# Optimization experiments

Hardware: AMD Instinct MI355X
Metric: run time of the kernel (lower is better)

Reference implementation:

```python
import jax, jax.numpy as jnp
import numpy as np
import math

D_MODEL = 1024
N_HEADS = 16
D_HEAD = D_MODEL // N_HEADS
WINDOW_LEN = 128
DILATION = 4
SEQ = 3072
BATCH = 1


def setup_inputs() -> dict:
    key = jax.random.key(0)
    ks = jax.random.split(key, 10)
    def xavier(k, shape):
        fan_out, fan_in = shape
        lim = math.sqrt(6.0 / (fan_in + fan_out))
        return jax.random.uniform(k, shape, jnp.float32, -lim, lim)
    return {
        "x": jax.random.normal(ks[0], (SEQ, BATCH, D_MODEL), jnp.float32),
        "beta": 0.1 * jax.random.normal(ks[1], (N_HEADS,), jnp.float32),
        "Wq": xavier(ks[2], (D_MODEL, D_MODEL)),
        "bq": jnp.zeros((D_MODEL,), jnp.float32),
        "Wk": xavier(ks[3], (D_MODEL, D_MODEL)),
        "bk": jnp.zeros((D_MODEL,), jnp.float32),
        "Wv": xavier(ks[4], (D_MODEL, D_MODEL)),
        "bv": jnp.zeros((D_MODEL,), jnp.float32),
        "Wo": xavier(ks[5], (D_MODEL, D_MODEL)),
        "bo": jnp.zeros((D_MODEL,), jnp.float32),
    }


def _causal_windowed_bias(seq_len):
    # allowed iff 0 <= (i-j), (i-j)//dilation < window_len, (i-j) % dilation == 0
    idx = jnp.arange(seq_len)
    diff = idx[:, None] - idx[None, :]
    allowed = (diff >= 0) & (diff // DILATION < WINDOW_LEN) & (diff % DILATION == 0)
    return jnp.where(allowed, 0.0, -jnp.inf).astype(jnp.float32)  # [S, S]


def reference(x, beta, Wq, bq, Wk, bk, Wv, bv, Wo, bo):
    s, b, d = x.shape
    # projections: nn.Linear => x @ W.T + b
    def split_heads(t):  # [s, b, h*dh] -> [b, h, s, dh]
        return t.reshape(s, b, N_HEADS, D_HEAD).transpose(1, 2, 0, 3)
    q = split_heads(x @ Wq.T + bq)
    k = split_heads(x @ Wk.T + bk)
    v = split_heads(x @ Wv.T + bv)
    # beta scaling folded into q, attention uses scale=1.0
    q = q / (math.sqrt(D_HEAD) * jnp.exp(beta)[None, :, None, None])
    bias = _causal_windowed_bias(s)  # [S, S]
    scores = jnp.einsum('bhsd,bhtd->bhst', q, k) + bias
    attn = jax.nn.softmax(scores, axis=-1)
    ctx = jnp.einsum('bhst,bhtd->bhsd', attn, v)  # [b, h, s, dh]
    ctx = ctx.transpose(2, 0, 1, 3).reshape(s, b, d)  # [s, b, d_model]
    return ctx @ Wo.T + bo
```

## Files before the change

kernel.cpp:

```cpp
#include <hip/hip_runtime.h>
#include <math.h>

#define SEQ   3072
#define DM    1024
#define NH    16
#define DH    64
#define WIN   128
#define DIL   4
#define TSUB  768

typedef __attribute__((ext_vector_type(8))) short    short8;
typedef __attribute__((ext_vector_type(8))) _Float16 half8;
typedef __attribute__((ext_vector_type(4))) float    floatx4;

__device__ __forceinline__ float bf2f(unsigned short u) {
    return __uint_as_float(((unsigned)u) << 16);
}
__device__ __forceinline__ unsigned short f2bf(float f) {
    unsigned u = __float_as_uint(f);
    return (unsigned short)((u + 0x7FFFu + ((u >> 16) & 1u)) >> 16);
}
__device__ __forceinline__ unsigned short f2h(float f) {
    _Float16 h = (_Float16)f;
    return __builtin_bit_cast(unsigned short, h);
}

__device__ __forceinline__ void gload_lds16(const void* g, void* l) {
    __builtin_amdgcn_global_load_lds(
        (const __attribute__((address_space(1))) void*)g,
        (__attribute__((address_space(3))) void*)l, 16, 0, 0);
}

__global__ __launch_bounds__(256) void convert_kernel(
    const float* __restrict__ x,  const float* __restrict__ Wq,
    const float* __restrict__ Wk, const float* __restrict__ Wv,
    const float* __restrict__ Wo,
    ushort* __restrict__ xb,  ushort* __restrict__ Wqb,
    ushort* __restrict__ Wkb, ushort* __restrict__ Wvb,
    ushort* __restrict__ Wob)
{
    const float* s; ushort* d; int n;
    switch (blockIdx.y) {
        case 0: s = x;  d = xb;  n = SEQ * DM; break;
        case 1: s = Wq; d = Wqb; n = DM * DM;  break;
        case 2: s = Wk; d = Wkb; n = DM * DM;  break;
        case 3: s = Wv; d = Wvb; n = DM * DM;  break;
        default: s = Wo; d = Wob; n = DM * DM; break;
    }
    int i = (blockIdx.x * 256 + threadIdx.x) * 4;
    if (i >= n) return;
    float4 v = *(const float4*)&s[i];
    ushort4 o = { f2bf(v.x), f2bf(v.y), f2bf(v.z), f2bf(v.w) };
    *(ushort4*)&d[i] = o;
}

struct QkvSmem {
    ushort As[128][64];
    ushort Bs[64][64];
};

template<bool QSCALE>
__device__ __forceinline__ void gemm_qkv_body(QkvSmem& sm,
                                              const ushort* __restrict__ A,
                                              const ushort* __restrict__ W,
                                              const float* __restrict__ bias,
                                              const float* __restrict__ beta,
                                              ushort* __restrict__ C,
                                              int bx, int by)
{
    const int tid  = threadIdx.x;
    const int lane = tid & 63, w = tid >> 6;
    const int ln15 = lane & 15, quad = lane >> 4;
    const int wm = w >> 1, wn = w & 1;

    const int arow = tid >> 1;
    const int sh   = tid & 1;
    const int ska  = (arow >> 1) & 7;
    const ushort* aG = A + (size_t)(by * 128 + arow) * DM + sh * 32;
    ushort* aL[4];
#pragma unroll
    for (int c = 0; c < 4; ++c) {
        int pos = (4 * sh + c) ^ ska;
        aL[c] = &sm.As[arow][pos * 8];
    }

    const int brow = tid >> 2;
    const int sq   = tid & 3;
    const int skb  = (brow >> 1) & 7;
    const ushort* bG = W + (size_t)(bx * 64 + brow) * DM + sq * 16;
    ushort* bL[2];
#pragma unroll
    for (int c = 0; c < 2; ++c) {
        int pos = (2 * sq + c) ^ skb;
        bL[c] = &sm.Bs[brow][pos * 8];
    }

    const floatx4 zero = {0.f, 0.f, 0.f, 0.f};
    floatx4 acc[4][2];
#pragma unroll
    for (int i = 0; i < 4; ++i)
#pragma unroll
        for (int j = 0; j < 2; ++j) acc[i][j] = zero;

    short8 ra[4], rb[2];
#pragma unroll
    for (int c = 0; c < 4; ++c) ra[c] = *(const short8*)(aG + 8 * c);
#pragma unroll
    for (int c = 0; c < 2; ++c) rb[c] = *(const short8*)(bG + 8 * c);
#pragma unroll
    for (int c = 0; c < 4; ++c) *(short8*)aL[c] = ra[c];
#pragma unroll
    for (int c = 0; c < 2; ++c) *(short8*)bL[c] = rb[c];
    __syncthreads();

    const int rf = (ln15 >> 1) & 7;
#pragma unroll 2
    for (int k = 0; k < 16; ++k) {
        if (k < 15) {
            const ushort* aN = aG + (k + 1) * 64;
            const ushort* bN = bG + (k + 1) * 64;
#pragma unroll
            for (int c = 0; c < 4; ++c) ra[c] = *(const short8*)(aN + 8 * c);
#pragma unroll
            for (int c = 0; c < 2; ++c) rb[c] = *(const short8*)(bN + 8 * c);
        }
#pragma unroll
        for (int s = 0; s < 2; ++s) {
            short8 af[4], bf[2];
#pragma unroll
            for (int i = 0; i < 4; ++i)
                af[i] = *(const short8*)&sm.As[wm * 64 + i * 16 + ln15][((s * 4 + quad) ^ rf) * 8];
#pragma unroll
            for (int j = 0; j < 2; ++j)
                bf[j] = *(const short8*)&sm.Bs[wn * 32 + j * 16 + ln15][((s * 4 + quad) ^ rf) * 8];
#pragma unroll
            for (int i = 0; i < 4; ++i)
#pragma unroll
                for (int j = 0; j < 2; ++j)
                    acc[i][j] = __builtin_amdgcn_mfma_f32_16x16x32_bf16(af[i], bf[j], acc[i][j], 0, 0, 0);
        }
        __syncthreads();
        if (k < 15) {
#pragma unroll
            for (int c = 0; c < 4; ++c) *(short8*)aL[c] = ra[c];
#pragma unroll
            for (int c = 0; c < 2; ++c) *(short8*)bL[c] = rb[c];
        }
        __syncthreads();
    }

#pragma unroll
    for (int j = 0; j < 2; ++j) {
        const int col = bx * 64 + wn * 32 + j * 16 + ln15;
        const float b = bias[col];
        const float scale = QSCALE ? 0.125f * __expf(-beta[col >> 6]) : 1.0f;
#pragma unroll
        for (int i = 0; i < 4; ++i) {
            const int row0 = by * 128 + wm * 64 + i * 16 + quad * 4;
#pragma unroll
            for (int rg = 0; rg < 4; ++rg) {
                float vv = (acc[i][j][rg] + b) * scale;
                C[(size_t)(row0 + rg) * DM + col] = f2bf(vv);
            }
        }
    }
}

__global__ __launch_bounds__(256, 4) void qkv_kernel(
    const ushort* __restrict__ xb,
    const ushort* __restrict__ Wqb, const float* __restrict__ bq,
    const ushort* __restrict__ Wkb, const float* __restrict__ bk,
    const ushort* __restrict__ Wvb, const float* __restrict__ bv,
    const float* __restrict__ beta,
    ushort* __restrict__ q, ushort* __restrict__ k, ushort* __restrict__ v)
{
    __shared__ QkvSmem sm;
    const int z = blockIdx.z;
    const ushort* W = (z == 0) ? Wqb : (z == 1) ? Wkb : Wvb;
    const float*  b = (z == 0) ? bq  : (z == 1) ? bk  : bv;
    ushort*       C = (z == 0) ? q   : (z == 1) ? k   : v;
    if (z == 0)
        gemm_qkv_body<true >(sm, xb, W, b, beta, C, blockIdx.x, blockIdx.y);
    else
        gemm_qkv_body<false>(sm, xb, W, b, nullptr, C, blockIdx.x, blockIdx.y);
}

__global__ __launch_bounds__(256) void out_kernel(
    const ushort* __restrict__ ctxb, const ushort* __restrict__ Wob,
    const float* __restrict__ bo, float* __restrict__ out)
{
    __shared__ ushort As[64][64];
    __shared__ ushort Bs[64][64];

    const int tid  = threadIdx.x;
    const int lane = tid & 63, w = tid >> 6;
    const int ln15 = lane & 15, quad = lane >> 4;
    const int wm = w >> 1, wn = w & 1;
    const int bx = blockIdx.x, by = blockIdx.y;

    const int srow = tid >> 2;
    const int sq   = tid & 3;
    const int sk   = (srow >> 1) & 7;
    const ushort* aG = ctxb + (size_t)(by * 64 + srow) * DM + sq * 16;
    const ushort* bG = Wob  + (size_t)(bx * 64 + srow) * DM + sq * 16;
    ushort* aL[2]; ushort* bL[2];
#pragma unroll
    for (int c = 0; c < 2; ++c) {
        int pos = (2 * sq + c) ^ sk;
        aL[c] = &As[srow][pos * 8];
        bL[c] = &Bs[srow][pos * 8];
    }

    const floatx4 zero = {0.f, 0.f, 0.f, 0.f};
    floatx4 acc[2][2];
#pragma unroll
    for (int i = 0; i < 2; ++i)
#pragma unroll
        for (int j = 0; j < 2; ++j) acc[i][j] = zero;

    short8 ra[2], rb[2];
#pragma unroll
    for (int c = 0; c < 2; ++c) {
        ra[c] = *(const short8*)(aG + 8 * c);
        rb[c] = *(const short8*)(bG + 8 * c);
    }
#pragma unroll
    for (int c = 0; c < 2; ++c) { *(short8*)aL[c] = ra[c]; *(short8*)bL[c] = rb[c]; }
    __syncthreads();

    const int rf = (ln15 >> 1) & 7;
#pragma unroll 2
    for (int k = 0; k < 16; ++k) {
        if (k < 15) {
            const ushort* aN = aG + (k + 1) * 64;
            const ushort* bN = bG + (k + 1) * 64;
#pragma unroll
            for (int c = 0; c < 2; ++c) {
                ra[c] = *(const short8*)(aN + 8 * c);
                rb[c] = *(const short8*)(bN + 8 * c);
            }
        }
#pragma unroll
        for (int s = 0; s < 2; ++s) {
            short8 af[2], bf[2];
#pragma unroll
            for (int i = 0; i < 2; ++i)
                af[i] = *(const short8*)&As[wm * 32 + i * 16 + ln15][((s * 4 + quad) ^ rf) * 8];
#pragma unroll
            for (int j = 0; j < 2; ++j)
                bf[j] = *(const short8*)&Bs[wn * 32 + j * 16 + ln15][((s * 4 + quad) ^ rf) * 8];
#pragma unroll
            for (int i = 0; i < 2; ++i)
#pragma unroll
                for (int j = 0; j < 2; ++j)
                    acc[i][j] = __builtin_amdgcn_mfma_f32_16x16x32_bf16(af[i], bf[j], acc[i][j], 0, 0, 0);
        }
        __syncthreads();
        if (k < 15) {
#pragma unroll
            for (int c = 0; c < 2; ++c) { *(short8*)aL[c] = ra[c]; *(short8*)bL[c] = rb[c]; }
        }
        __syncthreads();
    }

#pragma unroll
    for (int j = 0; j < 2; ++j) {
        const int col = bx * 64 + wn * 32 + j * 16 + ln15;
        const float b = bo[col];
#pragma unroll
        for (int i = 0; i < 2; ++i) {
            const int row0 = by * 64 + wm * 32 + i * 16 + quad * 4;
#pragma unroll
            for (int rg = 0; rg < 4; ++rg)
                out[(size_t)(row0 + rg) * DM + col] = acc[i][j][rg] + b;
        }
    }
}

struct AttnSmem {
    union {
        ushort Ks[192 * 64];
        ushort Vt[6 * 4 * 64 * 8];
    } u;
    float S[32][195];
    float Rsum[32];
};

__global__ __launch_bounds__(256) void attn_kernel(
    const ushort* __restrict__ q, const ushort* __restrict__ k,
    const ushort* __restrict__ v, ushort* __restrict__ ctx)
{
    __shared__ AttnSmem sm;

    const int tid  = threadIdx.x;
    const int lane = tid & 63, w = tid >> 6;
    const int ln15 = lane & 15, quad = lane >> 4;
    const int t0   = blockIdx.x * 32;
    const int r    = blockIdx.y;
    const int h    = blockIdx.z;
    const int hoff = h * DH;

    {
        const int kr = lane >> 3;
        const int swz = ((lane & 7) ^ kr) * 8;
#pragma unroll
        for (int ci = w * 6; ci < w * 6 + 6; ++ci) {
            int key = ci * 8 + kr;
            long grow = 4L * (t0 - 160 + key) + r;
            gload_lds16(k + grow * DM + hoff + swz, &sm.u.Ks[ci * 512]);
        }
    }

    const int qt = w >> 1;
    short8 qf0, qf1;
    {
        int qrow = qt * 16 + ln15;
        const ushort* gq = q + (4L * (t0 + qrow) + r) * DM + hoff + quad * 8;
        qf0 = *(const short8*)gq;
        qf1 = *(const short8*)(gq + 32);
    }

    short8 vreg[6];
#pragma unroll
    for (int it = 0; it < 6; ++it) {
        int idx = it * 256 + tid;
        int key = idx >> 3, d0 = (idx & 7) * 8;
        long grow = 4L * (t0 - 160 + key) + r;
        vreg[it] = *(const short8*)(v + grow * DM + hoff + d0);
    }

    __syncthreads();

    {
        const floatx4 zero = {0.f, 0.f, 0.f, 0.f};
        const int kt0 = (w & 1) * 6;
        const int lb  = ln15 & 7;
#pragma unroll
        for (int kk2 = 0; kk2 < 6; ++kk2) {
            const int kt  = kt0 + kk2;
            const int key = kt * 16 + ln15;
            short8 b0 = *(const short8*)&sm.u.Ks[key * 64 + ((quad ^ lb) << 3)];
            short8 b1 = *(const short8*)&sm.u.Ks[key * 64 + (((4 + quad) ^ lb) << 3)];
            floatx4 acc = zero;
            acc = __builtin_amdgcn_mfma_f32_16x16x32_bf16(qf0, b0, acc, 0, 0, 0);
            acc = __builtin_amdgcn_mfma_f32_16x16x32_bf16(qf1, b1, acc, 0, 0, 0);
            const int tp = t0 - 160 + key;
#pragma unroll
            for (int rg = 0; rg < 4; ++rg) {
                int qrow = qt * 16 + quad * 4 + rg;
                int tq = t0 + qrow;
                bool ok = (tp >= 0) && (tp <= tq) && (tp > tq - WIN);
                sm.S[qrow][key] = ok ? acc[rg] : -1e30f;
            }
        }
    }

    __syncthreads();

#pragma unroll
    for (int it = 0; it < 6; ++it) {
        int idx = it * 256 + tid;
        int key = idx >> 3, d0 = (idx & 7) * 8;
        int kc = key >> 5, qd = (key >> 3) & 3, jj = key & 7;
        short8 sv = vreg[it];
#pragma unroll
        for (int u = 0; u < 8; ++u) {
            int dim = d0 + u, dt = dim >> 4, ln = dim & 15;
            sm.u.Vt[(kc * 4 + dt) * 512 + (qd * 16 + ln) * 8 + jj] =
                f2h(bf2f((unsigned short)sv[u]));
        }
    }

    {
        const int sq = tid >> 3, part = tid & 7;
        float m = -1e30f;
#pragma unroll
        for (int j = 0; j < 24; ++j) m = fmaxf(m, sm.S[sq][part + 8 * j]);
#pragma unroll
        for (int o = 1; o < 8; o <<= 1) m = fmaxf(m, __shfl_xor(m, o));
        float sum = 0.f;
#pragma unroll
        for (int j = 0; j < 24; ++j) {
            int ks = part + 8 * j;
            float e = __expf(sm.S[sq][ks] - m);
            sm.S[sq][ks] = e;
            sum += e;
        }
#pragma unroll
        for (int o = 1; o < 8; o <<= 1) sum += __shfl_xor(sum, o);
        if (part == 0) sm.Rsum[sq] = 1.0f / sum;
    }

    __syncthreads();

    {
        const floatx4 zero = {0.f, 0.f, 0.f, 0.f};
        const int qtp = w & 1, dh = w >> 1;
        floatx4 o0 = zero, o1 = zero;
#pragma unroll
        for (int kc = 0; kc < 6; ++kc) {
            const float* ps = &sm.S[qtp * 16 + ln15][kc * 32 + quad * 8];
            half8 pa;
#pragma unroll
            for (int u = 0; u < 8; ++u) pa[u] = (_Float16)ps[u];
            half8 vb0 = *(const half8*)&sm.u.Vt[(kc * 4 + dh * 2 + 0) * 512 + lane * 8];
            half8 vb1 = *(const half8*)&sm.u.Vt[(kc * 4 + dh * 2 + 1) * 512 + lane * 8];
            o0 = __builtin_amdgcn_mfma_f32_16x16x32_f16(pa, vb0, o0, 0, 0, 0);
            o1 = __builtin_amdgcn_mfma_f32_16x16x32_f16(pa, vb1, o1, 0, 0, 0);
        }
#pragma unroll
        for (int rg = 0; rg < 4; ++rg) {
            int qrow = qtp * 16 + quad * 4 + rg;
            float rs = sm.Rsum[qrow];
            long orow = 4L * (t0 + qrow) + r;
            ushort* cp = ctx + orow * DM + hoff + dh * 32 + ln15;
            cp[0]  = f2bf(o0[rg] * rs);
            cp[16] = f2bf(o1[rg] * rs);
        }
    }
}

extern "C" void kernel_launch(void* const* d_in, const int* in_sizes, int n_in,
                              void* d_out, int out_size, void* d_ws, size_t ws_size,
                              hipStream_t stream)
{
    const float* x    = (const float*)d_in[0];
    const float* beta = (const float*)d_in[1];
    const float* Wq   = (const float*)d_in[2];
    const float* bq   = (const float*)d_in[3];
    const float* Wk   = (const float*)d_in[4];
    const float* bk   = (const float*)d_in[5];
    const float* Wv   = (const float*)d_in[6];
    const float* bv   = (const float*)d_in[7];
    const float* Wo   = (const float*)d_in[8];
    const float* bo   = (const float*)d_in[9];

    ushort* qb   = (ushort*)d_ws;
    ushort* kb   = qb   + (size_t)SEQ * DM;
    ushort* vb   = kb   + (size_t)SEQ * DM;
    ushort* ctxb = vb   + (size_t)SEQ * DM;
    ushort* xb   = ctxb + (size_t)SEQ * DM;
    ushort* Wqb  = xb   + (size_t)SEQ * DM;
    ushort* Wkb  = Wqb  + (size_t)DM * DM;
    ushort* Wvb  = Wkb  + (size_t)DM * DM;
    ushort* Wob  = Wvb  + (size_t)DM * DM;
    float*  out  = (float*)d_out;

    dim3 gcv(SEQ * DM / 4 / 256, 5);
    convert_kernel<<<gcv, 256, 0, stream>>>(x, Wq, Wk, Wv, Wo, xb, Wqb, Wkb, Wvb, Wob);

    dim3 gqkv(DM / 64, SEQ / 128, 3);
    qkv_kernel<<<gqkv, 256, 0, stream>>>(xb, Wqb, bq, Wkb, bk, Wvb, bv, beta, qb, kb, vb);

    dim3 gattn(TSUB / 32, DIL, NH);
    attn_kernel<<<gattn, 256, 0, stream>>>(qb, kb, vb, ctxb);

    dim3 gout(DM / 64, SEQ / 64);
    out_kernel<<<gout, 256, 0, stream>>>(ctxb, Wob, bo, out);
}
```

Before: 172.4 us.

## Use direct global-to-LDS loads with double-buffered shared tiles in GEMMs

Both projection GEMM kernels now stage tiles through a direct global-to-LDS load helper (gload_lds16) into two shared-memory buffers, and swap buffers each k-step. This drops the register round trip and one of the two barriers per iteration. The XOR swizzle moves to the global source address, so the LDS write pattern matches the existing fragment reads. Shared memory use doubles, so the occupancy hint drops to 3 blocks.

```diff
diff --git a/kernel.cpp b/kernel.cpp
--- a/kernel.cpp
+++ b/kernel.cpp
@@ -55,8 +55,8 @@
 }
 
 struct QkvSmem {
-    ushort As[128][64];
-    ushort Bs[64][64];
+    ushort As[2][128][64];
+    ushort Bs[2][64][64];
 };
 
 template<bool QSCALE>
@@ -73,26 +73,20 @@
     const int ln15 = lane & 15, quad = lane >> 4;
     const int wm = w >> 1, wn = w & 1;
 
-    const int arow = tid >> 1;
-    const int sh   = tid & 1;
-    const int ska  = (arow >> 1) & 7;
-    const ushort* aG = A + (size_t)(by * 128 + arow) * DM + sh * 32;
-    ushort* aL[4];
-#pragma unroll
-    for (int c = 0; c < 4; ++c) {
-        int pos = (4 * sh + c) ^ ska;
-        aL[c] = &sm.As[arow][pos * 8];
-    }
-
-    const int brow = tid >> 2;
-    const int sq   = tid & 3;
-    const int skb  = (brow >> 1) & 7;
-    const ushort* bG = W + (size_t)(bx * 64 + brow) * DM + sq * 16;
-    ushort* bL[2];
-#pragma unroll
-    for (int c = 0; c < 2; ++c) {
-        int pos = (2 * sq + c) ^ skb;
-        bL[c] = &sm.Bs[brow][pos * 8];
+    const int rl = lane >> 3, cl = lane & 7;
+    const ushort* aRow[4];
+#pragma unroll
+    for (int i = 0; i < 4; ++i) {
+        int row   = w * 32 + 8 * i + rl;
+        int chunk = cl ^ ((row >> 1) & 7);
+        aRow[i] = A + (size_t)(by * 128 + row) * DM + chunk * 8;
+    }
+    const ushort* bRow[2];
+#pragma unroll
+    for (int i = 0; i < 2; ++i) {
+        int row   = w * 16 + 8 * i + rl;
+        int chunk = cl ^ ((row >> 1) & 7);
+        bRow[i] = W + (size_t)(bx * 64 + row) * DM + chunk * 8;
     }
 
     const floatx4 zero = {0.f, 0.f, 0.f, 0.f};
@@ -102,49 +96,37 @@
 #pragma unroll
         for (int j = 0; j < 2; ++j) acc[i][j] = zero;
 
-    short8 ra[4], rb[2];
-#pragma unroll
-    for (int c = 0; c < 4; ++c) ra[c] = *(const short8*)(aG + 8 * c);
-#pragma unroll
-    for (int c = 0; c < 2; ++c) rb[c] = *(const short8*)(bG + 8 * c);
-#pragma unroll
-    for (int c = 0; c < 4; ++c) *(short8*)aL[c] = ra[c];
-#pragma unroll
-    for (int c = 0; c < 2; ++c) *(short8*)bL[c] = rb[c];
+#pragma unroll
+    for (int i = 0; i < 4; ++i) gload_lds16(aRow[i], &sm.As[0][w * 32 + 8 * i][0]);
+#pragma unroll
+    for (int i = 0; i < 2; ++i) gload_lds16(bRow[i], &sm.Bs[0][w * 16 + 8 * i][0]);
     __syncthreads();
 
     const int rf = (ln15 >> 1) & 7;
 #pragma unroll 2
-    for (int k = 0; k < 16; ++k) {
-        if (k < 15) {
-            const ushort* aN = aG + (k + 1) * 64;
-            const ushort* bN = bG + (k + 1) * 64;
-#pragma unroll
-            for (int c = 0; c < 4; ++c) ra[c] = *(const short8*)(aN + 8 * c);
-#pragma unroll
-            for (int c = 0; c < 2; ++c) rb[c] = *(const short8*)(bN + 8 * c);
+    for (int t = 0; t < 16; ++t) {
+        const int cur = t & 1, nxt = cur ^ 1;
+        if (t < 15) {
+            const int ko = (t + 1) * 64;
+#pragma unroll
+            for (int i = 0; i < 4; ++i) gload_lds16(aRow[i] + ko, &sm.As[nxt][w * 32 + 8 * i][0]);
+#pragma unroll
+            for (int i = 0; i < 2; ++i) gload_lds16(bRow[i] + ko, &sm.Bs[nxt][w * 16 + 8 * i][0]);
         }
 #pragma unroll
         for (int s = 0; s < 2; ++s) {
             short8 af[4], bf[2];
 #pragma unroll
             for (int i = 0; i < 4; ++i)
-                af[i] = *(const short8*)&sm.As[wm * 64 + i * 16 + ln15][((s * 4 + quad) ^ rf) * 8];
+                af[i] = *(const short8*)&sm.As[cur][wm * 64 + i * 16 + ln15][((s * 4 + quad) ^ rf) * 8];
 #pragma unroll
             for (int j = 0; j < 2; ++j)
-                bf[j] = *(const short8*)&sm.Bs[wn * 32 + j * 16 + ln15][((s * 4 + quad) ^ rf) * 8];
+                bf[j] = *(const short8*)&sm.Bs[cur][wn * 32 + j * 16 + ln15][((s * 4 + quad) ^ rf) * 8];
 #pragma unroll
             for (int i = 0; i < 4; ++i)
 #pragma unroll
                 for (int j = 0; j < 2; ++j)
                     acc[i][j] = __builtin_amdgcn_mfma_f32_16x16x32_bf16(af[i], bf[j], acc[i][j], 0, 0, 0);
-        }
-        __syncthreads();
-        if (k < 15) {
-#pragma unroll
-            for (int c = 0; c < 4; ++c) *(short8*)aL[c] = ra[c];
-#pragma unroll
-            for (int c = 0; c < 2; ++c) *(short8*)bL[c] = rb[c];
         }
         __syncthreads();
     }
@@ -166,7 +148,7 @@
     }
 }
 
-__global__ __launch_bounds__(256, 4) void qkv_kernel(
+__global__ __launch_bounds__(256, 3) void qkv_kernel(
     const ushort* __restrict__ xb,
     const ushort* __restrict__ Wqb, const float* __restrict__ bq,
     const ushort* __restrict__ Wkb, const float* __restrict__ bk,
@@ -185,12 +167,12 @@
         gemm_qkv_body<false>(sm, xb, W, b, nullptr, C, blockIdx.x, blockIdx.y);
 }
 
-__global__ __launch_bounds__(256) void out_kernel(
+__global__ __launch_bounds__(256, 3) void out_kernel(
     const ushort* __restrict__ ctxb, const ushort* __restrict__ Wob,
     const float* __restrict__ bo, float* __restrict__ out)
 {
-    __shared__ ushort As[64][64];
-    __shared__ ushort Bs[64][64];
+    __shared__ ushort As[2][64][64];
+    __shared__ ushort Bs[2][64][64];
 
     const int tid  = threadIdx.x;
     const int lane = tid & 63, w = tid >> 6;
@@ -198,17 +180,14 @@
     const int wm = w >> 1, wn = w & 1;
     const int bx = blockIdx.x, by = blockIdx.y;
 
-    const int srow = tid >> 2;
-    const int sq   = tid & 3;
-    const int sk   = (srow >> 1) & 7;
-    const ushort* aG = ctxb + (size_t)(by * 64 + srow) * DM + sq * 16;
-    const ushort* bG = Wob  + (size_t)(bx * 64 + srow) * DM + sq * 16;
-    ushort* aL[2]; ushort* bL[2];
-#pragma unroll
-    for (int c = 0; c < 2; ++c) {
-        int pos = (2 * sq + c) ^ sk;
-        aL[c] = &As[srow][pos * 8];
-        bL[c] = &Bs[srow][pos * 8];
+    const int rl = lane >> 3, cl = lane & 7;
+    const ushort* aRow[2]; const ushort* bRow[2];
+#pragma unroll
+    for (int i = 0; i < 2; ++i) {
+        int row   = w * 16 + 8 * i + rl;
+        int chunk = cl ^ ((row >> 1) & 7);
+        aRow[i] = ctxb + (size_t)(by * 64 + row) * DM + chunk * 8;
+        bRow[i] = Wob  + (size_t)(bx * 64 + row) * DM + chunk * 8;
     }
 
     const floatx4 zero = {0.f, 0.f, 0.f, 0.f};
@@ -218,26 +197,23 @@
 #pragma unroll
         for (int j = 0; j < 2; ++j) acc[i][j] = zero;
 
-    short8 ra[2], rb[2];
-#pragma unroll
-    for (int c = 0; c < 2; ++c) {
-        ra[c] = *(const short8*)(aG + 8 * c);
-        rb[c] = *(const short8*)(bG + 8 * c);
-    }
-#pragma unroll
-    for (int c = 0; c < 2; ++c) { *(short8*)aL[c] = ra[c]; *(short8*)bL[c] = rb[c]; }
+#pragma unroll
+    for (int i = 0; i < 2; ++i) {
+        gload_lds16(aRow[i], &As[0][w * 16 + 8 * i][0]);
+        gload_lds16(bRow[i], &Bs[0][w * 16 + 8 * i][0]);
+    }
     __syncthreads();
 
     const int rf = (ln15 >> 1) & 7;
 #pragma unroll 2
-    for (int k = 0; k < 16; ++k) {
-        if (k < 15) {
-            const ushort* aN = aG + (k + 1) * 64;
-            const ushort* bN = bG + (k + 1) * 64;
-#pragma unroll
-            for (int c = 0; c < 2; ++c) {
-                ra[c] = *(const short8*)(aN + 8 * c);
-                rb[c] = *(const short8*)(bN + 8 * c);
+    for (int t = 0; t < 16; ++t) {
+        const int cur = t & 1, nxt = cur ^ 1;
+        if (t < 15) {
+            const int ko = (t + 1) * 64;
+#pragma unroll
+            for (int i = 0; i < 2; ++i) {
+                gload_lds16(aRow[i] + ko, &As[nxt][w * 16 + 8 * i][0]);
+                gload_lds16(bRow[i] + ko, &Bs[nxt][w * 16 + 8 * i][0]);
             }
         }
 #pragma unroll
@@ -245,20 +221,15 @@
             short8 af[2], bf[2];
 #pragma unroll
             for (int i = 0; i < 2; ++i)
-                af[i] = *(const short8*)&As[wm * 32 + i * 16 + ln15][((s * 4 + quad) ^ rf) * 8];
+                af[i] = *(const short8*)&As[cur][wm * 32 + i * 16 + ln15][((s * 4 + quad) ^ rf) * 8];
 #pragma unroll
             for (int j = 0; j < 2; ++j)
-                bf[j] = *(const short8*)&Bs[wn * 32 + j * 16 + ln15][((s * 4 + quad) ^ rf) * 8];
+                bf[j] = *(const short8*)&Bs[cur][wn * 32 + j * 16 + ln15][((s * 4 + quad) ^ rf) * 8];
 #pragma unroll
             for (int i = 0; i < 2; ++i)
 #pragma unroll
                 for (int j = 0; j < 2; ++j)
                     acc[i][j] = __builtin_amdgcn_mfma_f32_16x16x32_bf16(af[i], bf[j], acc[i][j], 0, 0, 0);
-        }
-        __syncthreads();
-        if (k < 15) {
-#pragma unroll
-            for (int c = 0; c < 2; ++c) { *(short8*)aL[c] = ra[c]; *(short8*)bL[c] = rb[c]; }
         }
         __syncthreads();
     }
```

New measurement: 165.0 us. -4.2%, faster.
